# Kernel optimization log

Hardware: AMD Instinct MI355X
Metric: run time of the kernel (lower is better)

The kernel has to match this reference:

```python
import jax, jax.numpy as jnp
import numpy as np

NUM_HEADS = 32
HEAD_DIM = 512
EPS = 1e-12  # torch F.normalize eps


def setup_inputs() -> dict:
    key = jax.random.key(0)
    k1, k2, k3, k4, k5 = jax.random.split(key, 5)
    B, C, H, W = 32, 256, 64, 64
    return {
        "X": jax.random.normal(k1, (B, C, H, W), dtype=jnp.float32),
        "qkv_w": jax.random.normal(k2, (3 * HEAD_DIM, C), dtype=jnp.float32) * 0.02,
        "qkv_b": jax.random.normal(k3, (3 * HEAD_DIM,), dtype=jnp.float32) * 0.02,
        "proj_w": jax.random.normal(k4, (C, HEAD_DIM), dtype=jnp.float32) * 0.02,
        "proj_b": jax.random.normal(k5, (C,), dtype=jnp.float32) * 0.02,
    }


def _l2norm_axis1(x):
    # torch F.normalize(x, dim=1): x / max(||x||_2, eps)
    n = jnp.sqrt(jnp.sum(x * x, axis=1, keepdims=True))
    return x / jnp.maximum(n, EPS)


def reference(X, qkv_w, qkv_b, proj_w, proj_b):
    B, C, H, W = X.shape
    # 1x1 conv == channel matmul: [B,3*hd,H,W]
    qkv = jnp.einsum('bchw,oc->bohw', X, qkv_w) + qkv_b[None, :, None, None]
    # reshape to (B, 3, num_heads, head_dim, L) where L = H*W // num_heads
    qkv = qkv.reshape(B, 3, NUM_HEADS, HEAD_DIM, -1)
    q, k, v = qkv[:, 0], qkv[:, 1], qkv[:, 2]  # [B, nh, hd, L]
    # normalize across the num_heads axis (dim=1), as in the original code
    q = _l2norm_axis1(q)
    k = _l2norm_axis1(k)
    # attn = q^T @ k : [B, nh, L, L]
    attn = jnp.einsum('bhdl,bhdm->bhlm', q, k)
    attn = jax.nn.softmax(attn, axis=-1)
    # output = v @ attn^T : [B, nh, hd, L]
    out = jnp.einsum('bhdm,bhlm->bhdl', v, attn)
    out = out.reshape(B, HEAD_DIM, H, W)
    # proj 1x1 conv back to C channels
    out = jnp.einsum('bdhw,cd->bchw', out, proj_w) + proj_b[None, :, None, None]
    return out
```

## Files before the change

### kernel.cpp

```cpp
#include <hip/hip_runtime.h>
#include <stdint.h>


typedef float     f32x4   __attribute__((ext_vector_type(4)));
typedef short     bf16x8  __attribute__((ext_vector_type(8)));
typedef float     floatx4 __attribute__((ext_vector_type(4)));
typedef uint16_t  ushortx8 __attribute__((ext_vector_type(8)));
typedef uint16_t  ushortx4 __attribute__((ext_vector_type(4)));

#define DEVI static __device__ __forceinline__

DEVI float bf2f(uint16_t u) { union { uint32_t i; float f; } x; x.i = ((uint32_t)u) << 16; return x.f; }
DEVI uint16_t f2bf(float f) {
  union { float f; uint32_t i; } x; x.f = f;
  uint32_t r = x.i + 0x7fff + ((x.i >> 16) & 1);
  return (uint16_t)(r >> 16);
}

DEVI void gload16(const void* g, void* l) {
  __builtin_amdgcn_global_load_lds((const __attribute__((address_space(1))) void*)g,
                                   (__attribute__((address_space(3))) void*)l, 16, 0, 0);
}

DEVI float redmax16(float v) {
  v = fmaxf(v, __shfl_xor(v, 1)); v = fmaxf(v, __shfl_xor(v, 2));
  v = fmaxf(v, __shfl_xor(v, 4)); v = fmaxf(v, __shfl_xor(v, 8));
  return v;
}
DEVI float redsum16(float v) {
  v += __shfl_xor(v, 1); v += __shfl_xor(v, 2);
  v += __shfl_xor(v, 4); v += __shfl_xor(v, 8);
  return v;
}

__global__ __launch_bounds__(256) void k_transpose_x(const float* __restrict__ X,
                                                     uint16_t* __restrict__ Xt) {
  __shared__ float tile[64][65];
  int t = threadIdx.x;
  int st = blockIdx.x, ct = blockIdx.y, b = blockIdx.z;
  int row = t >> 2, cq = t & 3;
  const float* src = X + ((size_t)(b * 256 + ct * 64 + row)) * 4096 + st * 64 + cq * 16;
#pragma unroll
  for (int k = 0; k < 4; ++k) {
    floatx4 v = *(const floatx4*)(src + k * 4);
    tile[row][cq * 16 + k * 4 + 0] = v[0];
    tile[row][cq * 16 + k * 4 + 1] = v[1];
    tile[row][cq * 16 + k * 4 + 2] = v[2];
    tile[row][cq * 16 + k * 4 + 3] = v[3];
  }
  __syncthreads();
  int srow = t >> 2, oq = t & 3;
  ushortx8 o0, o1;
#pragma unroll
  for (int k = 0; k < 8; ++k) o0[k] = f2bf(tile[oq * 16 + k][srow]);
#pragma unroll
  for (int k = 0; k < 8; ++k) o1[k] = f2bf(tile[oq * 16 + 8 + k][srow]);
  uint16_t* dst = Xt + ((size_t)(b * 4096 + st * 64 + srow)) * 256 + ct * 64 + oq * 16;
  *(ushortx8*)dst = o0;
  *(ushortx8*)(dst + 8) = o1;
}

__global__ __launch_bounds__(256) void k_cvt_bf16(const float* __restrict__ src,
                                                  uint16_t* __restrict__ dst, int n) {
  int i = (blockIdx.x * 256 + threadIdx.x) * 4;
  if (i >= n) return;
  floatx4 v = *(const floatx4*)(src + i);
  ushortx4 o;
  o[0] = f2bf(v[0]); o[1] = f2bf(v[1]); o[2] = f2bf(v[2]); o[3] = f2bf(v[3]);
  *(ushortx4*)(dst + i) = o;
}

__global__ __launch_bounds__(256) void k_qkv_gemm(const uint16_t* __restrict__ W,
                                                  const uint16_t* __restrict__ Xt,
                                                  const float* __restrict__ bias_g,
                                                  uint16_t* __restrict__ qkv) {
  __shared__ __align__(16) union {
    uint16_t ab[2][128 * 64];
    uint16_t c[128 * 136];
  } sm;
  uint16_t* As = sm.ab[0];
  uint16_t* Bs = sm.ab[1];
  int t = threadIdx.x, lane = t & 63, wave = t >> 6;
  int ot = blockIdx.x, st = blockIdx.y, b = blockIdx.z;
  int wr = wave >> 1, wc = wave & 1;
  f32x4 acc[4][4] = {};
  int srow = lane >> 3;
  int sc_us = ((((lane & 7) * 16) ^ ((srow & 7) << 4)) >> 1);
  const uint16_t* Ag = W + (size_t)(ot * 128 + wave * 8 + srow) * 256;
  const uint16_t* Bg = Xt + ((size_t)(b * 4096 + st * 128 + wave * 8 + srow)) * 256;

  for (int kc = 0; kc < 4; ++kc) {
    __syncthreads();
#pragma unroll
    for (int c = 0; c < 4; ++c) {
      gload16(Ag + (size_t)(c * 32) * 256 + kc * 64 + sc_us, &As[(c * 32 + wave * 8) * 64]);
      gload16(Bg + (size_t)(c * 32) * 256 + kc * 64 + sc_us, &Bs[(c * 32 + wave * 8) * 64]);
    }
    __syncthreads();
#pragma unroll
    for (int kk = 0; kk < 2; ++kk) {
      bf16x8 a[4], bw[4];
#pragma unroll
      for (int i = 0; i < 4; ++i) {
        int r = wr * 64 + i * 16 + (lane & 15);
        a[i] = *(const bf16x8*)&As[r * 64 + ((kk * 32 + (lane >> 4) * 8) ^ ((r & 7) << 3))];
      }
#pragma unroll
      for (int j = 0; j < 4; ++j) {
        int r = wc * 64 + j * 16 + (lane & 15);
        bw[j] = *(const bf16x8*)&Bs[r * 64 + ((kk * 32 + (lane >> 4) * 8) ^ ((r & 7) << 3))];
      }
#pragma unroll
      for (int i = 0; i < 4; ++i)
#pragma unroll
        for (int j = 0; j < 4; ++j)
          acc[i][j] = __builtin_amdgcn_mfma_f32_16x16x32_bf16(a[i], bw[j], acc[i][j], 0, 0, 0);
    }
  }
  int o0 = ot * 128 + wr * 64;
  float bv[4][4];
#pragma unroll
  for (int i = 0; i < 4; ++i)
#pragma unroll
    for (int r = 0; r < 4; ++r) bv[i][r] = bias_g[o0 + i * 16 + (lane >> 4) * 4 + r];
  __syncthreads();
#pragma unroll
  for (int i = 0; i < 4; ++i)
#pragma unroll
    for (int j = 0; j < 4; ++j)
#pragma unroll
      for (int r = 0; r < 4; ++r) {
        int ol = wr * 64 + i * 16 + (lane >> 4) * 4 + r;
        int sl2 = wc * 64 + j * 16 + (lane & 15);
        sm.c[ol * 136 + sl2] = f2bf(acc[i][j][r] + bv[i][r]);
      }
  __syncthreads();
  uint16_t* outb = qkv + ((size_t)b * 1536 + ot * 128) * 4096 + st * 128;
  int rrow = t >> 4, rcol = (t & 15) * 8;
#pragma unroll
  for (int p = 0; p < 8; ++p) {
    int row = p * 16 + rrow;
    ushortx8 v = *(ushortx8*)&sm.c[row * 136 + rcol];
    *(ushortx8*)(outb + (size_t)row * 4096 + rcol) = v;
  }
}

__global__ __launch_bounds__(256) void k_scales(const uint16_t* __restrict__ qkv,
                                                float* __restrict__ scaleB) {
  int t = threadIdx.x;
  int sc = blockIdx.x, g = blockIdx.y, b = blockIdx.z;
  const uint16_t* base = qkv + ((size_t)(b * 1536 + g * 512)) * 4096;
  float* sb = scaleB + (size_t)b * 524288 + (size_t)g * 65536;
  int c16 = t >> 4, so = t & 15;
  int s = sc * 128 + so * 8;
  float ss[8] = {};
  for (int h = 0; h < 32; ++h) {
    ushortx8 v = *(const ushortx8*)(base + ((size_t)(h * 16 + c16)) * 4096 + s);
#pragma unroll
    for (int j = 0; j < 8; ++j) { float f = bf2f(v[j]); ss[j] += f * f; }
  }
  floatx4 o0, o1;
#pragma unroll
  for (int j = 0; j < 4; ++j) o0[j] = 1.0f / fmaxf(sqrtf(ss[j]), 1e-12f);
#pragma unroll
  for (int j = 0; j < 4; ++j) o1[j] = 1.0f / fmaxf(sqrtf(ss[4 + j]), 1e-12f);
  *(floatx4*)(sb + c16 * 4096 + s) = o0;
  *(floatx4*)(sb + c16 * 4096 + s + 4) = o1;
}

__global__ __launch_bounds__(512, 4) void k_attn(const uint16_t* __restrict__ qkv,
                                                 const float* __restrict__ scaleB,
                                                 uint16_t* OtAll) {
  __shared__ __align__(16) uint16_t stage[10240];
  __shared__ __align__(16) uint16_t Pb[16384];
  __shared__ float rsum[128];
  int t = threadIdx.x, lane = t & 63, w = t >> 6;
  int h = blockIdx.x, b = blockIdx.y;
  const uint16_t* qg = qkv + ((size_t)(b * 1536) + h * 16) * 4096;
  const uint16_t* kg = qkv + ((size_t)(b * 1536) + 512 + h * 16) * 4096;
  const float* sq = scaleB + (size_t)b * 524288;
  const float* sk = sq + 65536;
  uint16_t* QT = stage;
  uint16_t* KT = stage + 5120;

  int sl = t & 127;
  int sb8 = t >> 7;

  f32x4 accs[8] = {};
  for (int kc = 0; kc < 16; ++kc) {
    const uint16_t* qrow = qg + (size_t)kc * 4096 + sl;
    const uint16_t* krow = kg + (size_t)kc * 4096 + sl;
    const float* sqr = sq + kc * 4096 + sl;
    const float* skr = sk + kc * 4096 + sl;
    ushortx8 oq, ok;
#pragma unroll
    for (int j = 0; j < 8; ++j) {
      int soff = (sb8 * 8 + j) * 128;
      oq[j] = f2bf(bf2f(qrow[soff]) * sqr[soff]);
      ok[j] = f2bf(bf2f(krow[soff]) * skr[soff]);
    }
    __syncthreads();
    int lidx = sl * 40 + sb8 * 8;
    *(ushortx8*)&QT[lidx] = oq;
    *(ushortx8*)&KT[lidx] = ok;
    __syncthreads();
    int ra = w * 16 + (lane & 15);
    bf16x8 aq = *(const bf16x8*)&QT[ra * 40 + (lane >> 4) * 8];
#pragma unroll
    for (int mf = 0; mf < 8; ++mf) {
      int rm = mf * 16 + (lane & 15);
      bf16x8 bk = *(const bf16x8*)&KT[rm * 40 + (lane >> 4) * 8];
      accs[mf] = __builtin_amdgcn_mfma_f32_16x16x32_bf16(aq, bk, accs[mf], 0, 0, 0);
    }
  }

#pragma unroll
  for (int r = 0; r < 4; ++r) {
    float mx = accs[0][r];
#pragma unroll
    for (int mf = 1; mf < 8; ++mf) mx = fmaxf(mx, accs[mf][r]);
    mx = redmax16(mx);
    float sum = 0.f;
#pragma unroll
    for (int mf = 0; mf < 8; ++mf) {
      float e = __expf(accs[mf][r] - mx);
      accs[mf][r] = e;
      sum += e;
    }
    sum = redsum16(sum);
    int l = w * 16 + (lane >> 4) * 4 + r;
    if ((lane & 15) == 0) rsum[l] = 1.0f / sum;
#pragma unroll
    for (int mf = 0; mf < 8; ++mf) {
      int m = mf * 16 + (lane & 15);
      Pb[l * 128 + (m ^ ((l & 7) << 3))] = f2bf(accs[mf][r]);
    }
  }
  __syncthreads();

  const uint16_t* vg = qkv + ((size_t)(b * 1536) + 1024 + h * 16) * 4096;
  uint16_t* OtT = OtAll + (size_t)b * 6291456;
  uint16_t* Vt = stage;
  int vrow = lane >> 2;
  int vcol_us = ((((lane & 3) * 16) ^ ((vrow & 3) << 4)) >> 1);

#pragma unroll
  for (int lc = 0; lc < 2; ++lc) {
    f32x4 acco[2][2][4] = {};
    for (int mc = 0; mc < 4; ++mc) {
      bf16x8 bp[4];
#pragma unroll
      for (int lf = 0; lf < 4; ++lf) {
        int l = lc * 64 + lf * 16 + (lane & 15);
        bp[lf] = *(const bf16x8*)&Pb[l * 128 + ((mc * 32 + (lane >> 4) * 8) ^ ((l & 7) << 3))];
      }
#pragma unroll
      for (int half = 0; half < 2; ++half) {
        __syncthreads();
#pragma unroll
        for (int c = 0; c < 2; ++c) {
          int d = half * 256 + w * 32 + c * 16 + vrow;
          gload16(vg + (size_t)(d >> 5) * 4096 + (d & 31) * 128 + mc * 32 + vcol_us,
                  &Vt[(w * 32 + c * 16) * 32]);
        }
        __syncthreads();
#pragma unroll
        for (int df = 0; df < 2; ++df) {
          int rv = w * 32 + df * 16 + (lane & 15);
          bf16x8 av = *(const bf16x8*)&Vt[rv * 32 + (((lane >> 4) * 8) ^ ((rv & 3) << 3))];
#pragma unroll
          for (int lf = 0; lf < 4; ++lf)
            acco[half][df][lf] =
                __builtin_amdgcn_mfma_f32_16x16x32_bf16(av, bp[lf], acco[half][df][lf], 0, 0, 0);
        }
      }
    }
    float scl[4];
#pragma unroll
    for (int lf = 0; lf < 4; ++lf) scl[lf] = rsum[lc * 64 + lf * 16 + (lane & 15)];

    __syncthreads();
    uint16_t* patch = stage + w * 1056;
#pragma unroll
    for (int half = 0; half < 2; ++half) {
      uint16_t* obase = OtT + (size_t)(h * 16 + half * 8 + w) * 4096;
#pragma unroll
      for (int df = 0; df < 2; ++df) {
#pragma unroll
        for (int r = 0; r < 4; ++r) {
          int dlocal = (lane >> 4) * 4 + r;
#pragma unroll
          for (int lf = 0; lf < 4; ++lf)
            patch[dlocal * 66 + lf * 16 + (lane & 15)] = f2bf(acco[half][df][lf][r] * scl[lf]);
        }
        asm volatile("s_waitcnt lgkmcnt(0)" ::: "memory");
        __builtin_amdgcn_sched_barrier(0);
        int dl = lane >> 2, l8 = (lane & 3) * 16;
        uint16_t tmp[16];
#pragma unroll
        for (int e = 0; e < 8; ++e)
          *(uint32_t*)&tmp[e * 2] = *(const uint32_t*)&patch[dl * 66 + l8 + e * 2];
        uint16_t* gp = obase + (df * 16 + dl) * 128 + lc * 64 + l8;
        *(ushortx8*)gp = *(ushortx8*)&tmp[0];
        *(ushortx8*)(gp + 8) = *(ushortx8*)&tmp[8];
        asm volatile("s_waitcnt lgkmcnt(0)" ::: "memory");
        __builtin_amdgcn_sched_barrier(0);
      }
    }
  }
}

__global__ __launch_bounds__(256) void k_proj_gemm(const uint16_t* __restrict__ Wp,
                                                   const uint16_t* __restrict__ OtAll,
                                                   const float* __restrict__ bias_g,
                                                   float* __restrict__ outp) {
  __shared__ __align__(16) uint16_t As[128 * 64];
  __shared__ __align__(16) uint16_t Bs[128 * 64];
  int t = threadIdx.x, lane = t & 63, wave = t >> 6;
  int st = blockIdx.x, ct = blockIdx.y, b = blockIdx.z;
  int wr = wave >> 1, wc = wave & 1;
  f32x4 acc[4][4] = {};
  int srow = lane >> 3;
  int sc_us = ((((lane & 7) * 16) ^ ((srow & 7) << 4)) >> 1);
  const uint16_t* Ag = Wp + (size_t)(ct * 128 + wave * 8 + srow) * 512;
  const uint16_t* Ob = OtAll + (size_t)b * 6291456;

  for (int kc = 0; kc < 8; ++kc) {
    __syncthreads();
#pragma unroll
    for (int c = 0; c < 4; ++c)
      gload16(Ag + (size_t)(c * 32) * 512 + kc * 64 + sc_us, &As[(c * 32 + wave * 8) * 64]);
#pragma unroll
    for (int k = 0; k < 4; ++k) {
      int cid = k * 256 + t;
      int row = cid & 127, dd8 = cid >> 7;
      const uint16_t* src = Ob + (size_t)(kc * 64 + dd8 * 8) * 4096 + st * 128 + row;
      ushortx8 o;
#pragma unroll
      for (int j = 0; j < 8; ++j) o[j] = src[(size_t)j * 4096];
      *(ushortx8*)&Bs[row * 64 + ((dd8 * 8) ^ ((row & 7) << 3))] = o;
    }
    __syncthreads();
#pragma unroll
    for (int kk = 0; kk < 2; ++kk) {
      bf16x8 a[4], bw[4];
#pragma unroll
      for (int i = 0; i < 4; ++i) {
        int r = wr * 64 + i * 16 + (lane & 15);
        a[i] = *(const bf16x8*)&As[r * 64 + ((kk * 32 + (lane >> 4) * 8) ^ ((r & 7) << 3))];
      }
#pragma unroll
      for (int j = 0; j < 4; ++j) {
        int r = wc * 64 + j * 16 + (lane & 15);
        bw[j] = *(const bf16x8*)&Bs[r * 64 + ((kk * 32 + (lane >> 4) * 8) ^ ((r & 7) << 3))];
      }
#pragma unroll
      for (int i = 0; i < 4; ++i)
#pragma unroll
        for (int j = 0; j < 4; ++j)
          acc[i][j] = __builtin_amdgcn_mfma_f32_16x16x32_bf16(a[i], bw[j], acc[i][j], 0, 0, 0);
    }
  }
  int c0 = ct * 128 + wr * 64, s0 = st * 128 + wc * 64;
  float bv[4][4];
#pragma unroll
  for (int i = 0; i < 4; ++i)
#pragma unroll
    for (int r = 0; r < 4; ++r) bv[i][r] = bias_g[c0 + i * 16 + (lane >> 4) * 4 + r];
#pragma unroll
  for (int i = 0; i < 4; ++i)
#pragma unroll
    for (int j = 0; j < 4; ++j)
#pragma unroll
      for (int r = 0; r < 4; ++r) {
        int c = c0 + i * 16 + (lane >> 4) * 4 + r;
        int s = s0 + j * 16 + (lane & 15);
        outp[((size_t)b * 256 + c) * 4096 + s] = acc[i][j][r] + bv[i][r];
      }
}

extern "C" void kernel_launch(void* const* d_in, const int* in_sizes, int n_in,
                              void* d_out, int out_size, void* d_ws, size_t ws_size,
                              hipStream_t stream) {
  const float* X      = (const float*)d_in[0];
  const float* qkv_w  = (const float*)d_in[1];
  const float* qkv_b  = (const float*)d_in[2];
  const float* proj_w = (const float*)d_in[3];
  const float* proj_b = (const float*)d_in[4];
  float* outp = (float*)d_out;

  const size_t SZ_XT  = 2097152;
  const size_t SZ_QKV = 12582912;
  const size_t SZ_W   = 786432 + 262144;

  int NB = 0;
  const int cand[6] = {32, 16, 8, 4, 2, 1};
  for (int ci = 0; ci < 6; ++ci) {
    size_t need = SZ_W + (size_t)cand[ci] * (SZ_XT + SZ_QKV);
    if (need <= ws_size) { NB = cand[ci]; break; }
  }
  if (NB == 0) return;

  char* ws = (char*)d_ws;
  uint16_t* Wqb  = (uint16_t*)(ws);
  uint16_t* Wpb  = (uint16_t*)(ws + 786432);
  char*     gbuf = ws + SZ_W;
  uint16_t* Xt   = (uint16_t*)(gbuf);
  uint16_t* qkvb = (uint16_t*)(gbuf + (size_t)NB * SZ_XT);
  float*    scaleB = (float*)Xt;

  k_cvt_bf16<<<dim3(384), 256, 0, stream>>>(qkv_w, Wqb, 1536 * 256);
  k_cvt_bf16<<<dim3(128), 256, 0, stream>>>(proj_w, Wpb, 256 * 512);

  for (int b0 = 0; b0 < 32; b0 += NB) {
    const float* Xg   = X + (size_t)b0 * 256 * 4096;
    float*       outg = outp + (size_t)b0 * 256 * 4096;
    k_transpose_x<<<dim3(64, 4, NB), 256, 0, stream>>>(Xg, Xt);
    k_qkv_gemm<<<dim3(12, 32, NB), 256, 0, stream>>>(Wqb, Xt, qkv_b, qkvb);
    k_scales<<<dim3(32, 2, NB), 256, 0, stream>>>(qkvb, scaleB);
    k_attn<<<dim3(32, NB), 512, 0, stream>>>(qkvb, scaleB, qkvb );
    k_proj_gemm<<<dim3(32, 2, NB), 256, 0, stream>>>(Wpb, qkvb , proj_b, outg);
  }
}
```

Measured before the change: 578.3 us.

## Fuse q/k sum-of-squares into QKV GEMM epilogue and enlarge GEMM tile

```diff
diff --git a/kernel.cpp b/kernel.cpp
--- a/kernel.cpp
+++ b/kernel.cpp
@@ -70,32 +70,34 @@
   *(ushortx4*)(dst + i) = o;
 }
 
-__global__ __launch_bounds__(256) void k_qkv_gemm(const uint16_t* __restrict__ W,
+__global__ __launch_bounds__(512) void k_qkv_gemm(const uint16_t* __restrict__ W,
                                                   const uint16_t* __restrict__ Xt,
                                                   const float* __restrict__ bias_g,
-                                                  uint16_t* __restrict__ qkv) {
+                                                  uint16_t* __restrict__ qkv,
+                                                  float* __restrict__ gss) {
   __shared__ __align__(16) union {
-    uint16_t ab[2][128 * 64];
-    uint16_t c[128 * 136];
+    struct { uint16_t A[256 * 64]; uint16_t B[128 * 64]; } s;
+    struct { uint16_t c[128 * 136]; float ssl[16 * 128]; } e;
   } sm;
-  uint16_t* As = sm.ab[0];
-  uint16_t* Bs = sm.ab[1];
+  uint16_t* As = sm.s.A;
+  uint16_t* Bs = sm.s.B;
   int t = threadIdx.x, lane = t & 63, wave = t >> 6;
   int ot = blockIdx.x, st = blockIdx.y, b = blockIdx.z;
   int wr = wave >> 1, wc = wave & 1;
   f32x4 acc[4][4] = {};
   int srow = lane >> 3;
   int sc_us = ((((lane & 7) * 16) ^ ((srow & 7) << 4)) >> 1);
-  const uint16_t* Ag = W + (size_t)(ot * 128 + wave * 8 + srow) * 256;
+  const uint16_t* Ag = W + (size_t)(ot * 256 + wave * 8 + srow) * 256;
   const uint16_t* Bg = Xt + ((size_t)(b * 4096 + st * 128 + wave * 8 + srow)) * 256;
 
   for (int kc = 0; kc < 4; ++kc) {
     __syncthreads();
 #pragma unroll
-    for (int c = 0; c < 4; ++c) {
-      gload16(Ag + (size_t)(c * 32) * 256 + kc * 64 + sc_us, &As[(c * 32 + wave * 8) * 64]);
-      gload16(Bg + (size_t)(c * 32) * 256 + kc * 64 + sc_us, &Bs[(c * 32 + wave * 8) * 64]);
-    }
+    for (int c = 0; c < 4; ++c)
+      gload16(Ag + (size_t)(c * 64) * 256 + kc * 64 + sc_us, &As[(c * 64 + wave * 8) * 64]);
+#pragma unroll
+    for (int c = 0; c < 2; ++c)
+      gload16(Bg + (size_t)(c * 64) * 256 + kc * 64 + sc_us, &Bs[(c * 64 + wave * 8) * 64]);
     __syncthreads();
 #pragma unroll
     for (int kk = 0; kk < 2; ++kk) {
@@ -117,55 +119,80 @@
           acc[i][j] = __builtin_amdgcn_mfma_f32_16x16x32_bf16(a[i], bw[j], acc[i][j], 0, 0, 0);
     }
   }
-  int o0 = ot * 128 + wr * 64;
+
+  int o0 = ot * 256 + wr * 64;
   float bv[4][4];
 #pragma unroll
   for (int i = 0; i < 4; ++i)
 #pragma unroll
     for (int r = 0; r < 4; ++r) bv[i][r] = bias_g[o0 + i * 16 + (lane >> 4) * 4 + r];
+  bool isqk = (ot < 4);
   __syncthreads();
 #pragma unroll
-  for (int i = 0; i < 4; ++i)
+  for (int k = 0; k < 4; ++k) sm.e.ssl[k * 512 + t] = 0.f;
+  __syncthreads();
+  if (isqk) {
 #pragma unroll
     for (int j = 0; j < 4; ++j)
 #pragma unroll
       for (int r = 0; r < 4; ++r) {
-        int ol = wr * 64 + i * 16 + (lane >> 4) * 4 + r;
-        int sl2 = wc * 64 + j * 16 + (lane & 15);
-        sm.c[ol * 136 + sl2] = f2bf(acc[i][j][r] + bv[i][r]);
-      }
+        float ssv = 0.f;
+#pragma unroll
+        for (int i = 0; i < 4; ++i) {
+          float v = acc[i][j][r] + bv[i][r];
+          ssv += v * v;
+        }
+        int c16 = (lane >> 4) * 4 + r;
+        int scol = wc * 64 + j * 16 + (lane & 15);
+        atomicAdd(&sm.e.ssl[c16 * 128 + scol], ssv);
+      }
+  }
   __syncthreads();
-  uint16_t* outb = qkv + ((size_t)b * 1536 + ot * 128) * 4096 + st * 128;
-  int rrow = t >> 4, rcol = (t & 15) * 8;
-#pragma unroll
-  for (int p = 0; p < 8; ++p) {
-    int row = p * 16 + rrow;
-    ushortx8 v = *(ushortx8*)&sm.c[row * 136 + rcol];
-    *(ushortx8*)(outb + (size_t)row * 4096 + rcol) = v;
-  }
-}
-
-__global__ __launch_bounds__(256) void k_scales(const uint16_t* __restrict__ qkv,
-                                                float* __restrict__ scaleB) {
-  int t = threadIdx.x;
-  int sc = blockIdx.x, g = blockIdx.y, b = blockIdx.z;
-  const uint16_t* base = qkv + ((size_t)(b * 1536 + g * 512)) * 4096;
-  float* sb = scaleB + (size_t)b * 524288 + (size_t)g * 65536;
-  int c16 = t >> 4, so = t & 15;
-  int s = sc * 128 + so * 8;
-  float ss[8] = {};
-  for (int h = 0; h < 32; ++h) {
-    ushortx8 v = *(const ushortx8*)(base + ((size_t)(h * 16 + c16)) * 4096 + s);
-#pragma unroll
-    for (int j = 0; j < 8; ++j) { float f = bf2f(v[j]); ss[j] += f * f; }
-  }
-  floatx4 o0, o1;
-#pragma unroll
-  for (int j = 0; j < 4; ++j) o0[j] = 1.0f / fmaxf(sqrtf(ss[j]), 1e-12f);
-#pragma unroll
-  for (int j = 0; j < 4; ++j) o1[j] = 1.0f / fmaxf(sqrtf(ss[4 + j]), 1e-12f);
-  *(floatx4*)(sb + c16 * 4096 + s) = o0;
-  *(floatx4*)(sb + c16 * 4096 + s + 4) = o1;
+#pragma unroll
+  for (int h2 = 0; h2 < 2; ++h2) {
+    if ((wr >> 1) == h2) {
+      int lr0 = (wr & 1) * 64;
+#pragma unroll
+      for (int i = 0; i < 4; ++i)
+#pragma unroll
+        for (int j = 0; j < 4; ++j)
+#pragma unroll
+          for (int r = 0; r < 4; ++r) {
+            int lrow = lr0 + i * 16 + (lane >> 4) * 4 + r;
+            int scol = wc * 64 + j * 16 + (lane & 15);
+            sm.e.c[lrow * 136 + scol] = f2bf(acc[i][j][r] + bv[i][r]);
+          }
+    }
+    __syncthreads();
+    uint16_t* outb = qkv + ((size_t)b * 1536 + ot * 256 + h2 * 128) * 4096 + st * 128;
+    int rrow = t >> 4, rcol = (t & 15) * 8;
+#pragma unroll
+    for (int p = 0; p < 4; ++p) {
+      int row = p * 32 + rrow;
+      ushortx8 v = *(ushortx8*)&sm.e.c[row * 136 + rcol];
+      *(ushortx8*)(outb + (size_t)row * 4096 + rcol) = v;
+    }
+    __syncthreads();
+  }
+  if (isqk) {
+    int g = ot >> 1;
+    float* gb = gss + (size_t)b * 131072 + g * 65536 + st * 128;
+#pragma unroll
+    for (int it = 0; it < 4; ++it) {
+      int idx = it * 512 + t;
+      int c16 = idx >> 7, scol = idx & 127;
+      atomicAdd(&gb[(size_t)c16 * 4096 + scol], sm.e.ssl[c16 * 128 + scol]);
+    }
+  }
+}
+
+__global__ __launch_bounds__(256) void k_ss2scale(float* __restrict__ gss, int n) {
+  int i = (blockIdx.x * 256 + threadIdx.x) * 4;
+  if (i >= n) return;
+  floatx4 v = *(const floatx4*)(gss + i);
+#pragma unroll
+  for (int j = 0; j < 4; ++j) v[j] = 1.0f / fmaxf(sqrtf(v[j]), 1e-12f);
+  *(floatx4*)(gss + i) = v;
 }
 
 __global__ __launch_bounds__(512, 4) void k_attn(const uint16_t* __restrict__ qkv,
@@ -178,7 +205,7 @@
   int h = blockIdx.x, b = blockIdx.y;
   const uint16_t* qg = qkv + ((size_t)(b * 1536) + h * 16) * 4096;
   const uint16_t* kg = qkv + ((size_t)(b * 1536) + 512 + h * 16) * 4096;
-  const float* sq = scaleB + (size_t)b * 524288;
+  const float* sq = scaleB + (size_t)b * 131072;
   const float* sk = sq + 65536;
   uint16_t* QT = stage;
   uint16_t* KT = stage + 5120;
@@ -391,12 +418,13 @@
 
   const size_t SZ_XT  = 2097152;
   const size_t SZ_QKV = 12582912;
+  const size_t SZ_SC  = 524288;
   const size_t SZ_W   = 786432 + 262144;
 
   int NB = 0;
   const int cand[6] = {32, 16, 8, 4, 2, 1};
   for (int ci = 0; ci < 6; ++ci) {
-    size_t need = SZ_W + (size_t)cand[ci] * (SZ_XT + SZ_QKV);
+    size_t need = SZ_W + (size_t)cand[ci] * (SZ_XT + SZ_QKV + SZ_SC);
     if (need <= ws_size) { NB = cand[ci]; break; }
   }
   if (NB == 0) return;
@@ -407,7 +435,7 @@
   char*     gbuf = ws + SZ_W;
   uint16_t* Xt   = (uint16_t*)(gbuf);
   uint16_t* qkvb = (uint16_t*)(gbuf + (size_t)NB * SZ_XT);
-  float*    scaleB = (float*)Xt;
+  float*    scaleB = (float*)(gbuf + (size_t)NB * (SZ_XT + SZ_QKV));
 
   k_cvt_bf16<<<dim3(384), 256, 0, stream>>>(qkv_w, Wqb, 1536 * 256);
   k_cvt_bf16<<<dim3(128), 256, 0, stream>>>(proj_w, Wpb, 256 * 512);
@@ -415,9 +443,10 @@
   for (int b0 = 0; b0 < 32; b0 += NB) {
     const float* Xg   = X + (size_t)b0 * 256 * 4096;
     float*       outg = outp + (size_t)b0 * 256 * 4096;
+    hipMemsetAsync(scaleB, 0, (size_t)NB * SZ_SC, stream);
     k_transpose_x<<<dim3(64, 4, NB), 256, 0, stream>>>(Xg, Xt);
-    k_qkv_gemm<<<dim3(12, 32, NB), 256, 0, stream>>>(Wqb, Xt, qkv_b, qkvb);
-    k_scales<<<dim3(32, 2, NB), 256, 0, stream>>>(qkvb, scaleB);
+    k_qkv_gemm<<<dim3(6, 32, NB), 512, 0, stream>>>(Wqb, Xt, qkv_b, qkvb, scaleB);
+    k_ss2scale<<<dim3(NB * 128), 256, 0, stream>>>(scaleB, NB * 131072);
     k_attn<<<dim3(32, NB), 512, 0, stream>>>(qkvb, scaleB, qkvb );
     k_proj_gemm<<<dim3(32, 2, NB), 256, 0, stream>>>(Wpb, qkvb , proj_b, outg);
   }
```

After: 666.7 us. 1.15x slower.
